# Performance work log

Hardware: AMD Instinct MI355X
Metric: run time of the kernel (lower is better)

## Reference

```python
import jax, jax.numpy as jnp
import numpy as np
import math

B, T, D_MODEL, N_HEADS, K_CONV = 2, 2048, 2048, 16, 4
HEAD_DIM = D_MODEL // N_HEADS
EPS_GN = 1e-5


def setup_inputs() -> dict:
    key = jax.random.key(0)
    ks = jax.random.split(key, 16)
    s = 0.02
    # gamma bias init per reset_parameters (decays 0.9..0.9999 per head)
    min_d, max_d = 0.9, 0.9999
    tgt = 1.0 - np.exp(np.linspace(math.log(1 - min_d), math.log(1 - max_d), N_HEADS))
    gamma_bias = np.log(tgt / (1 - tgt)).astype(np.float32)
    return {
        "x": jax.random.normal(ks[0], (B, T, D_MODEL), jnp.float32),
        "Wq": jax.random.normal(ks[1], (D_MODEL, D_MODEL), jnp.float32) * s,
        "Wk": jax.random.normal(ks[2], (D_MODEL, D_MODEL), jnp.float32) * s,
        "Wv": jax.random.normal(ks[3], (D_MODEL, D_MODEL), jnp.float32) * s,
        "Wo": jax.random.normal(ks[4], (D_MODEL, D_MODEL), jnp.float32) * s,
        "conv_w": jax.random.normal(ks[5], (D_MODEL, K_CONV), jnp.float32) * 0.1,
        "conv_b": jnp.zeros((D_MODEL,), jnp.float32),
        "Wig": jax.random.normal(ks[6], (D_MODEL, D_MODEL), jnp.float32) * s,
        "b_ig": jnp.zeros((D_MODEL,), jnp.float32),
        "Wog": jax.random.normal(ks[7], (D_MODEL, D_MODEL), jnp.float32) * s,
        "b_og": jnp.zeros((D_MODEL,), jnp.float32),
        "Wg": jnp.zeros((N_HEADS, D_MODEL), jnp.float32),
        "b_g": jnp.asarray(gamma_bias),
        "gn_w": jnp.ones((D_MODEL,), jnp.float32),
        "gn_b": jnp.zeros((D_MODEL,), jnp.float32),
        "mn_w": jnp.ones((D_MODEL,), jnp.float32),
        "mn_b": jnp.zeros((D_MODEL,), jnp.float32),
    }


def _group_norm(x2d, w, b, groups, eps):
    # x2d: [N, C], normalize per group of C//groups channels
    N, C = x2d.shape
    xg = x2d.reshape(N, groups, C // groups)
    mu = xg.mean(-1, keepdims=True)
    var = ((xg - mu) ** 2).mean(-1, keepdims=True)
    xn = ((xg - mu) * jax.lax.rsqrt(var + eps)).reshape(N, C)
    return xn * w + b


def _causal_depthwise_conv(x, w, b):
    # x: [B,T,C], w: [C,K], b: [C] -> [B,T,C] causal depthwise conv + silu
    xt = jnp.transpose(x, (0, 2, 1))  # [B,C,T]
    xp = jnp.pad(xt, ((0, 0), (0, 0), (K_CONV - 1, 0)))
    y = jax.lax.conv_general_dilated(
        xp, w[:, None, :], (1,), "VALID",
        feature_group_count=D_MODEL,
        dimension_numbers=("NCH", "OIH", "NCH"))
    y = y + b[None, :, None]
    return jax.nn.silu(jnp.transpose(y, (0, 2, 1)))


def _l2norm(t):
    n = jnp.sqrt(jnp.sum(t * t, axis=-1, keepdims=True))
    return t / jnp.maximum(n, 1e-12)


def reference(x, Wq, Wk, Wv, Wo, conv_w, conv_b, Wig, b_ig, Wog, b_og, Wg, b_g, gn_w, gn_b, mn_w, mn_b):
    Bq, Tq, C = x.shape
    x_conv = _causal_depthwise_conv(x, conv_w, conv_b)  # [B,T,C]

    q = _l2norm((x @ Wq.T).reshape(Bq, Tq, N_HEADS, HEAD_DIM))
    k = _l2norm((x @ Wk.T).reshape(Bq, Tq, N_HEADS, HEAD_DIM))
    v = (x @ Wv.T).reshape(Bq, Tq, N_HEADS, HEAD_DIM)

    input_gate = jax.nn.sigmoid(x_conv @ Wig.T + b_ig).reshape(Bq, Tq, N_HEADS, HEAD_DIM)
    gamma = jax.nn.sigmoid(x_conv @ Wg.T + b_g).reshape(Bq, Tq, N_HEADS, 1)

    # gated elementwise linear recurrence: h_t = gamma_t * h_{t-1} + i_t * (k_t * v_t)
    bterm = input_gate * k * v                       # [B,T,H,D]
    aterm = jnp.broadcast_to(gamma, bterm.shape)     # [B,T,H,D]

    def scan_op(c1, c2):
        a1, b1 = c1
        a2, b2 = c2
        return (a1 * a2, a2 * b1 + b2)

    _, mem = jax.lax.associative_scan(scan_op, (aterm, bterm), axis=1)
    next_rnn_state = mem[:, -1]

    mem_n = _group_norm(mem.reshape(Bq * Tq, D_MODEL), mn_w, mn_b, N_HEADS, EPS_GN)
    mem_n = mem_n.reshape(Bq, Tq, N_HEADS, HEAD_DIM)

    out = (mem_n * q).reshape(Bq * Tq, C)
    out = _group_norm(out, gn_w, gn_b, N_HEADS, EPS_GN).reshape(Bq, Tq, C)

    output_gate = jax.nn.sigmoid(x_conv @ Wog.T + b_og)
    out = (out * output_gate) @ Wo.T

    new_conv_cache = jnp.transpose(x, (0, 2, 1))[:, :, -(K_CONV - 1):]
    return out, next_rnn_state, new_conv_cache
```

## Files before the change

### kernel.cpp

```cpp
#include <hip/hip_runtime.h>
#include <math.h>

#define B_ 2
#define T_ 2048
#define D_ 2048
#define H_ 16
#define M_ 4096
#define TD_ (T_ * D_)
#define EPS_ 1e-5f
#define NC_ 64
#define CL_ 32

typedef __bf16 bf16x8 __attribute__((ext_vector_type(8)));
typedef float f32x4 __attribute__((ext_vector_type(4)));

__device__ __forceinline__ float sigm(float z) { return 1.f / (1.f + __expf(-z)); }

__device__ __forceinline__ ushort f2bf(float f) {
    union { float f; uint u; } x; x.f = f;
    uint r = x.u + 0x7fffu + ((x.u >> 16) & 1u);
    return (ushort)(r >> 16);
}
__device__ __forceinline__ float bflo(uint u) { union { uint u; float f; } x; x.u = u << 16; return x.f; }
__device__ __forceinline__ float bfhi(uint u) { union { uint u; float f; } x; x.u = u & 0xffff0000u; return x.f; }

__device__ __forceinline__ void gload_lds16(const void* g, void* l) {
    __builtin_amdgcn_global_load_lds((const __attribute__((address_space(1))) void*)g,
                                     (__attribute__((address_space(3))) void*)l, 16, 0, 0);
}

template <int IMM>
__device__ __forceinline__ bf16x8 dsr(uint addr) {
    int4 d;
    asm volatile("ds_read_b128 %0, %1 offset:%2" : "=v"(d) : "v"(addr), "n"(IMM));
    return __builtin_bit_cast(bf16x8, d);
}
#define SCB   __builtin_amdgcn_sched_barrier(0)
#define SBAR  __builtin_amdgcn_s_barrier()

__global__ __launch_bounds__(256) void cvtw_kernel(
    const float* __restrict__ Wq, const float* __restrict__ Wk, const float* __restrict__ Wv,
    const float* __restrict__ Wig, const float* __restrict__ Wog, const float* __restrict__ Wo,
    ushort* __restrict__ W6)
{
    const int z = blockIdx.y;
    const float* src = z == 0 ? Wq : z == 1 ? Wk : z == 2 ? Wv : z == 3 ? Wig : z == 4 ? Wog : Wo;
    const int i4 = (blockIdx.x * 256 + threadIdx.x) * 4;
    float4 f = *(const float4*)(src + i4);
    ushort4 o; o.x = f2bf(f.x); o.y = f2bf(f.y); o.z = f2bf(f.z); o.w = f2bf(f.w);
    *(ushort4*)(W6 + (size_t)z * ((size_t)D_ * D_) + i4) = o;
}

__global__ __launch_bounds__(256) void conv_kernel(
    const float* __restrict__ x, const float* __restrict__ cw, const float* __restrict__ cb,
    ushort* __restrict__ xb, ushort* __restrict__ xcb, float* __restrict__ cach)
{
    const int idx = blockIdx.x * 256 + threadIdx.x;
    const int c = idx & (D_ - 1);
    const int t = (idx >> 11) & (T_ - 1);
    const int b = idx >> 22;
    const float* w = cw + c * 4;
    const float x3 = x[idx];
    float a = cb[c] + w[3] * x3;
    if (t >= 1) a += w[2] * x[idx - D_];
    if (t >= 2) a += w[1] * x[idx - 2 * D_];
    if (t >= 3) a += w[0] * x[idx - 3 * D_];
    xb[idx] = f2bf(x3);
    xcb[idx] = f2bf(a * sigm(a));
    if (t >= T_ - 3) cach[((size_t)b * D_ + c) * 3 + (t - (T_ - 3))] = x3;
}

template <bool BF16OUT>
__device__ __forceinline__ void gemm256_body(
    const ushort* __restrict__ A, const ushort* __restrict__ Bw,
    ushort* __restrict__ Cb, float* __restrict__ Cf, int bx, int by)
{
    extern __shared__ char smem[];
    const int tid = threadIdx.x;
    const int lane = tid & 63, wid = tid >> 6;
    const int wm = wid >> 1, wn = wid & 1;
    const int l15 = lane & 15, l4 = lane >> 4;
    const int brow = by * 256, bcol = bx * 128;

    const int srow = tid >> 3;
    const int scol = ((tid & 7) * 8) ^ (((tid >> 3) & 7) << 3);
    const uint sldso = (uint)tid * 16;

    f32x4 acc[4][4] = {};

    #define STAGE6(bufo, k0)                                                         \
        do {                                                                         \
            _Pragma("unroll")                                                        \
            for (int j = 0; j < 4; ++j)                                              \
                gload_lds16(A + (size_t)(brow + j * 64 + srow) * D_ + ((k0) + scol), \
                            smem + (bufo) + j * 8192 + sldso);                       \
            _Pragma("unroll")                                                        \
            for (int j = 0; j < 2; ++j)                                              \
                gload_lds16(Bw + (size_t)(bcol + j * 64 + srow) * D_ + ((k0) + scol),\
                            smem + (bufo) + 32768u + j * 8192 + sldso);              \
        } while (0)

    STAGE6(0u, 0);
    STAGE6(49152u, 64);
    asm volatile("s_waitcnt vmcnt(6)" ::: "memory");
    SBAR; SCB;

    const uint r7  = (uint)((l15 & 7) << 4);
    const uint ca0 = (uint)(l4 * 16) ^ r7;
    const uint ca1 = (uint)(64 + l4 * 16) ^ r7;
    const uint arow = (uint)(wm * 64 + l15) * 128u;
    const uint brw  = 32768u + (uint)(wn * 64 + l15) * 128u;
    const uint ldsbase = (uint)(size_t)smem;

    #pragma unroll 2
    for (int t = 0; t < 32; ++t) {
        const uint bo = ldsbase + (uint)(t & 1) * 49152u;
        const uint ab0 = bo + arow + ca0, ab1 = bo + arow + ca1;
        const uint bb0 = bo + brw + ca0,  bb1 = bo + brw + ca1;
        bf16x8 a0[8], b0[4], b1[4];
        a0[0] = dsr<0>(ab0);        a0[1] = dsr<0>(ab1);
        a0[2] = dsr<2048>(ab0);     a0[3] = dsr<2048>(ab1);
        a0[4] = dsr<4096>(ab0);     a0[5] = dsr<4096>(ab1);
        a0[6] = dsr<6144>(ab0);     a0[7] = dsr<6144>(ab1);
        b0[0] = dsr<0>(bb0);        b0[1] = dsr<0>(bb1);
        b0[2] = dsr<2048>(bb0);     b0[3] = dsr<2048>(bb1);
        b1[0] = dsr<4096>(bb0);     b1[1] = dsr<4096>(bb1);
        b1[2] = dsr<6144>(bb0);     b1[3] = dsr<6144>(bb1);
        asm volatile("s_waitcnt lgkmcnt(4)" ::: "memory");
        SCB;
        __builtin_amdgcn_s_setprio(1);
        #pragma unroll
        for (int ks = 0; ks < 2; ++ks)
            #pragma unroll
            for (int m = 0; m < 4; ++m)
                #pragma unroll
                for (int n = 0; n < 2; ++n)
                    acc[m][n] = __builtin_amdgcn_mfma_f32_16x16x32_bf16(
                        a0[m * 2 + ks], b0[n * 2 + ks], acc[m][n], 0, 0, 0);
        SCB;
        __builtin_amdgcn_s_setprio(0);
        asm volatile("s_waitcnt lgkmcnt(0)" ::: "memory");
        SCB;
        __builtin_amdgcn_s_setprio(1);
        #pragma unroll
        for (int ks = 0; ks < 2; ++ks)
            #pragma unroll
            for (int m = 0; m < 4; ++m)
                #pragma unroll
                for (int n = 0; n < 2; ++n)
                    acc[m][2 + n] = __builtin_amdgcn_mfma_f32_16x16x32_bf16(
                        a0[m * 2 + ks], b1[n * 2 + ks], acc[m][2 + n], 0, 0, 0);
        SCB;
        __builtin_amdgcn_s_setprio(0);
        if (t <= 29) {
            const uint bo2 = (uint)(t & 1) * 49152u;
            STAGE6(bo2, (t + 2) * 64);
        }
        if (t < 31) {
            if (t < 30) asm volatile("s_waitcnt vmcnt(6)" ::: "memory");
            else        asm volatile("s_waitcnt vmcnt(0)" ::: "memory");
            SBAR; SCB;
        }
    }
    #undef STAGE6

    #pragma unroll
    for (int m = 0; m < 4; ++m)
        #pragma unroll
        for (int n = 0; n < 4; ++n) {
            const int row = brow + wm * 64 + m * 16 + l4 * 4;
            const int col = bcol + wn * 64 + n * 16 + l15;
            #pragma unroll
            for (int r = 0; r < 4; ++r) {
                if (BF16OUT) Cb[(size_t)(row + r) * D_ + col] = f2bf(acc[m][n][r]);
                else         Cf[(size_t)(row + r) * D_ + col] = acc[m][n][r];
            }
        }
}

__global__ __launch_bounds__(512, 2) void gemm5_kernel(
    const ushort* __restrict__ xb, const ushort* __restrict__ xcb,
    const ushort* __restrict__ W6, ushort* __restrict__ Obuf)
{
    const int g = (blockIdx.z * 16 + blockIdx.y) * 16 + blockIdx.x;
    const int ns = (g & 7) * 160 + (g >> 3);
    const int z = ns >> 8, rem = ns & 255, by = rem >> 4, bx = rem & 15;
    const ushort* Aop = (z < 3) ? xb : xcb;
    gemm256_body<true>(Aop, W6 + (size_t)z * ((size_t)D_ * D_),
                       Obuf + (size_t)z * ((size_t)M_ * D_), nullptr, bx, by);
}

__global__ __launch_bounds__(512, 2) void gemm_out_kernel(
    const ushort* __restrict__ gated, const ushort* __restrict__ W6, float* __restrict__ out)
{
    const int g = blockIdx.y * 16 + blockIdx.x;
    const int ns = (g & 7) * 32 + (g >> 3);
    const int by = ns >> 4, bx = ns & 15;
    gemm256_body<false>(gated, W6 + (size_t)5 * ((size_t)D_ * D_), nullptr, out, bx, by);
}

__global__ __launch_bounds__(256) void gamma_kernel(
    const ushort* __restrict__ xcb, const float* __restrict__ Wg,
    const float* __restrict__ bg, float* __restrict__ gamma)
{
    __shared__ ushort xs[8 * D_];
    const int tid = threadIdx.x;
    const int tok0 = blockIdx.x * 8;
    const uint4* gsrc = (const uint4*)(xcb + (size_t)tok0 * D_);
    #pragma unroll
    for (int j = 0; j < 8; ++j)
        ((uint4*)xs)[j * 256 + tid] = gsrc[j * 256 + tid];
    __syncthreads();
    const int tok = tid >> 5;
    const int h = (tid >> 1) & 15;
    const int half = tid & 1;
    const ushort* xr = xs + tok * D_ + half * 1024;
    const float* wr = Wg + (size_t)h * D_ + half * 1024;
    float acc = 0.f;
    #pragma unroll 4
    for (int i = 0; i < 1024; i += 8) {
        uint4 u = *(const uint4*)(xr + i);
        float4 w0 = *(const float4*)(wr + i);
        float4 w1 = *(const float4*)(wr + i + 4);
        acc += bflo(u.x) * w0.x + bfhi(u.x) * w0.y + bflo(u.y) * w0.z + bfhi(u.y) * w0.w;
        acc += bflo(u.z) * w1.x + bfhi(u.z) * w1.y + bflo(u.w) * w1.z + bfhi(u.w) * w1.w;
    }
    acc += __shfl_xor(acc, 1);
    if (!half) gamma[(size_t)(tok0 + tok) * H_ + h] = sigm(acc + bg[h]);
}

__global__ __launch_bounds__(64) void scanA_kernel(
    const ushort* __restrict__ kb, const ushort* __restrict__ vb,
    const ushort* __restrict__ igb, const float* __restrict__ big,
    const float* __restrict__ gam, float* __restrict__ Ab, float* __restrict__ Sb)
{
    const int l = threadIdx.x;
    const int ch = blockIdx.x, h = blockIdx.y, b = blockIdx.z;
    const int c0 = h * 128 + 2 * l;
    const float bg0 = big[c0], bg1 = big[c0 + 1];
    const float* g = gam + ((size_t)b * T_ + ch * CL_) * H_ + h;
    const size_t base0 = ((size_t)b * T_ + ch * CL_) * D_ + c0;
    float a = 1.f, sA = 0.f, sB = 0.f;
    for (int i = 0; i < CL_; ++i) {
        const size_t off = base0 + (size_t)i * D_;
        const uint ku = *(const uint*)(kb + off);
        const uint vu = *(const uint*)(vb + off);
        const uint iu = *(const uint*)(igb + off);
        const float k0 = bflo(ku), k1 = bfhi(ku);
        float ssq = k0 * k0 + k1 * k1;
        #pragma unroll
        for (int o = 1; o < 64; o <<= 1) ssq += __shfl_xor(ssq, o);
        const float sc = 1.f / fmaxf(sqrtf(ssq), 1e-12f);
        const float b0 = sigm(bflo(iu) + bg0) * (k0 * sc) * bflo(vu);
        const float b1 = sigm(bfhi(iu) + bg1) * (k1 * sc) * bfhi(vu);
        const float gv = g[(size_t)i * H_];
        sA = fmaf(gv, sA, b0);
        sB = fmaf(gv, sB, b1);
        a *= gv;
    }
    const size_t o = ((size_t)b * NC_ + ch) * D_ + c0;
    Ab[o] = a; Ab[o + 1] = a; Sb[o] = sA; Sb[o + 1] = sB;
}

__global__ __launch_bounds__(256) void scan2_kernel(
    const float* __restrict__ Ab, const float* __restrict__ Sb, float* __restrict__ carry)
{
    const int idx = blockIdx.x * 256 + threadIdx.x;
    const int b = idx >> 11, c = idx & (D_ - 1);
    float run = 0.f;
    #pragma unroll 8
    for (int ch = 0; ch < NC_; ++ch) {
        const size_t o = ((size_t)b * NC_ + ch) * D_ + c;
        carry[o] = run;
        run = fmaf(Ab[o], run, Sb[o]);
    }
}

__global__ __launch_bounds__(64) void scanB_kernel(
    const ushort* __restrict__ kb, const ushort* __restrict__ vb,
    const ushort* __restrict__ igb, const ushort* __restrict__ qb,
    const ushort* __restrict__ ogb, const float* __restrict__ big,
    const float* __restrict__ bog, const float* __restrict__ mnw,
    const float* __restrict__ mnb, const float* __restrict__ gnw,
    const float* __restrict__ gnb, const float* __restrict__ gam,
    const float* __restrict__ carry, ushort* __restrict__ gated,
    float* __restrict__ rnn)
{
    const int l = threadIdx.x;
    const int ch = blockIdx.x, h = blockIdx.y, b = blockIdx.z;
    const int c0 = h * 128 + 2 * l;
    const float bg0 = big[c0], bg1 = big[c0 + 1];
    const float bo0 = bog[c0], bo1 = bog[c0 + 1];
    const float mw0 = mnw[c0], mw1 = mnw[c0 + 1], mb0 = mnb[c0], mb1 = mnb[c0 + 1];
    const float gw0 = gnw[c0], gw1 = gnw[c0 + 1], gb0 = gnb[c0], gb1 = gnb[c0 + 1];
    const float* g = gam + ((size_t)b * T_ + ch * CL_) * H_ + h;
    const size_t base0 = ((size_t)b * T_ + ch * CL_) * D_ + c0;
    float m0 = carry[((size_t)b * NC_ + ch) * D_ + c0];
    float m1 = carry[((size_t)b * NC_ + ch) * D_ + c0 + 1];
    for (int i = 0; i < CL_; ++i) {
        const size_t off = base0 + (size_t)i * D_;
        const uint ku = *(const uint*)(kb + off);
        const uint vu = *(const uint*)(vb + off);
        const uint iu = *(const uint*)(igb + off);
        const uint qu = *(const uint*)(qb + off);
        const uint ou = *(const uint*)(ogb + off);
        const float k0 = bflo(ku), k1 = bfhi(ku);
        float ssq = k0 * k0 + k1 * k1;
        #pragma unroll
        for (int o = 1; o < 64; o <<= 1) ssq += __shfl_xor(ssq, o);
        const float sc = 1.f / fmaxf(sqrtf(ssq), 1e-12f);
        const float bt0 = sigm(bflo(iu) + bg0) * (k0 * sc) * bflo(vu);
        const float bt1 = sigm(bfhi(iu) + bg1) * (k1 * sc) * bfhi(vu);
        const float gv = g[(size_t)i * H_];
        m0 = fmaf(gv, m0, bt0);
        m1 = fmaf(gv, m1, bt1);
        const float q0 = bflo(qu), q1 = bfhi(qu);
        float r1 = m0 + m1, r2 = m0 * m0 + m1 * m1, r3 = q0 * q0 + q1 * q1;
        #pragma unroll
        for (int o = 1; o < 64; o <<= 1) {
            r1 += __shfl_xor(r1, o); r2 += __shfl_xor(r2, o); r3 += __shfl_xor(r3, o);
        }
        const float mu  = r1 * (1.f / 128.f);
        const float inv = 1.f / sqrtf(fmaxf(r2 * (1.f / 128.f) - mu * mu, 0.f) + EPS_);
        const float qsc = 1.f / fmaxf(sqrtf(r3), 1e-12f);
        const float ov0 = ((m0 - mu) * inv * mw0 + mb0) * (q0 * qsc);
        const float ov1 = ((m1 - mu) * inv * mw1 + mb1) * (q1 * qsc);
        float t1 = ov0 + ov1, t2 = ov0 * ov0 + ov1 * ov1;
        #pragma unroll
        for (int o = 1; o < 64; o <<= 1) { t1 += __shfl_xor(t1, o); t2 += __shfl_xor(t2, o); }
        const float mu2  = t1 * (1.f / 128.f);
        const float inv2 = 1.f / sqrtf(fmaxf(t2 * (1.f / 128.f) - mu2 * mu2, 0.f) + EPS_);
        const float g0 = ((ov0 - mu2) * inv2 * gw0 + gb0) * sigm(bflo(ou) + bo0);
        const float g1 = ((ov1 - mu2) * inv2 * gw1 + gb1) * sigm(bfhi(ou) + bo1);
        *(uint*)(gated + off) = (uint)f2bf(g0) | ((uint)f2bf(g1) << 16);
    }
    if (ch == NC_ - 1) {
        rnn[(size_t)b * D_ + c0] = m0;
        rnn[(size_t)b * D_ + c0 + 1] = m1;
    }
}

extern "C" void kernel_launch(void* const* d_in, const int* in_sizes, int n_in,
                              void* d_out, int out_size, void* d_ws, size_t ws_size,
                              hipStream_t stream)
{
    const float* x   = (const float*)d_in[0];
    const float* Wq  = (const float*)d_in[1];
    const float* Wk  = (const float*)d_in[2];
    const float* Wv  = (const float*)d_in[3];
    const float* Wo  = (const float*)d_in[4];
    const float* cw  = (const float*)d_in[5];
    const float* cb  = (const float*)d_in[6];
    const float* Wig = (const float*)d_in[7];
    const float* big = (const float*)d_in[8];
    const float* Wog = (const float*)d_in[9];
    const float* bog = (const float*)d_in[10];
    const float* Wg  = (const float*)d_in[11];
    const float* bg  = (const float*)d_in[12];
    const float* gnw = (const float*)d_in[13];
    const float* gnb = (const float*)d_in[14];
    const float* mnw = (const float*)d_in[15];
    const float* mnb = (const float*)d_in[16];

    char* ws = (char*)d_ws;
    ushort* W6   = (ushort*)ws;
    ushort* xb   = (ushort*)(ws + 50331648);
    ushort* xcb  = (ushort*)(ws + 50331648 + 16777216);
    ushort* Obuf = (ushort*)(ws + 50331648 + 2 * 16777216);
    float*  gam  = (float*)(ws + 167772160);
    ushort* gated= (ushort*)(ws + 167772160 + 1048576);
    float*  Ab   = (float*)(ws + 167772160 + 1048576 + 16777216);
    float*  Sb   = Ab + (size_t)B_ * NC_ * D_;
    float*  carry= Sb + (size_t)B_ * NC_ * D_;

    ushort* q    = Obuf;
    ushort* k    = Obuf + (size_t)M_ * D_;
    ushort* v    = Obuf + 2 * (size_t)M_ * D_;
    ushort* igp  = Obuf + 3 * (size_t)M_ * D_;
    ushort* ogp  = Obuf + 4 * (size_t)M_ * D_;

    float* out  = (float*)d_out;
    float* rnn  = out + (size_t)M_ * D_;
    float* cach = rnn + B_ * D_;

    (void)hipFuncSetAttribute((const void*)gemm5_kernel,
                              hipFuncAttributeMaxDynamicSharedMemorySize, 98304);
    (void)hipFuncSetAttribute((const void*)gemm_out_kernel,
                              hipFuncAttributeMaxDynamicSharedMemorySize, 98304);

    cvtw_kernel<<<dim3(4096, 6), 256, 0, stream>>>(Wq, Wk, Wv, Wig, Wog, Wo, W6);
    conv_kernel<<<dim3(M_ * D_ / 256), 256, 0, stream>>>(x, cw, cb, xb, xcb, cach);
    gemm5_kernel<<<dim3(16, 16, 5), 512, 98304, stream>>>(xb, xcb, W6, Obuf);
    gamma_kernel<<<dim3(M_ / 8), 256, 0, stream>>>(xcb, Wg, bg, gam);
    scanA_kernel<<<dim3(NC_, H_, B_), 64, 0, stream>>>(k, v, igp, big, gam, Ab, Sb);
    scan2_kernel<<<dim3(16), 256, 0, stream>>>(Ab, Sb, carry);
    scanB_kernel<<<dim3(NC_, H_, B_), 64, 0, stream>>>(k, v, igp, q, ogp, big, bog,
                                                       mnw, mnb, gnw, gnb, gam, carry,
                                                       gated, rnn);
    gemm_out_kernel<<<dim3(16, 16), 512, 98304, stream>>>(gated, W6, out);
}
```

Measured before the change: 416.3 us.

## Vectorize scan kernels to 8 channels per lane and shorten scan chunks

Each lane in the chunked-scan kernels now handles 8 contiguous channels with 128-bit bf16 loads and stores, and a wave covers 4 heads with 16-lane shuffle reductions instead of 64-lane ones. Chunk length drops from 32 to 8, giving 256 chunks. The per-chunk decay/state buffer is interleaved as float2 and stored channel-major. Workspace regions freed by earlier stages (xb, W6) are reused for the scan buffers and the gated output. The aim is fewer, wider memory transactions and shorter reduction chains, at the cost of a 4x longer serial carry pass in scan2, which now reads with strided, poorly coalesced access.

```diff
diff --git a/kernel.cpp b/kernel.cpp
--- a/kernel.cpp
+++ b/kernel.cpp
@@ -8,8 +8,8 @@
 #define M_ 4096
 #define TD_ (T_ * D_)
 #define EPS_ 1e-5f
-#define NC_ 64
-#define CL_ 32
+#define NC_ 256
+#define CL_ 8
 
 typedef __bf16 bf16x8 __attribute__((ext_vector_type(8)));
 typedef float f32x4 __attribute__((ext_vector_type(4)));
@@ -23,6 +23,13 @@
 }
 __device__ __forceinline__ float bflo(uint u) { union { uint u; float f; } x; x.u = u << 16; return x.f; }
 __device__ __forceinline__ float bfhi(uint u) { union { uint u; float f; } x; x.u = u & 0xffff0000u; return x.f; }
+
+__device__ __forceinline__ void unp8(uint4 u, float* f) {
+    f[0] = bflo(u.x); f[1] = bfhi(u.x); f[2] = bflo(u.y); f[3] = bfhi(u.y);
+    f[4] = bflo(u.z); f[5] = bfhi(u.z); f[6] = bflo(u.w); f[7] = bfhi(u.w);
+}
+#define RED16(v) do { v += __shfl_xor(v, 1); v += __shfl_xor(v, 2); \
+                      v += __shfl_xor(v, 4); v += __shfl_xor(v, 8); } while (0)
 
 __device__ __forceinline__ void gload_lds16(const void* g, void* l) {
     __builtin_amdgcn_global_load_lds((const __attribute__((address_space(1))) void*)g,
@@ -232,47 +239,55 @@
 __global__ __launch_bounds__(64) void scanA_kernel(
     const ushort* __restrict__ kb, const ushort* __restrict__ vb,
     const ushort* __restrict__ igb, const float* __restrict__ big,
-    const float* __restrict__ gam, float* __restrict__ Ab, float* __restrict__ Sb)
+    const float* __restrict__ gam, float2* __restrict__ AS)
 {
     const int l = threadIdx.x;
-    const int ch = blockIdx.x, h = blockIdx.y, b = blockIdx.z;
-    const int c0 = h * 128 + 2 * l;
-    const float bg0 = big[c0], bg1 = big[c0 + 1];
+    const int ch = blockIdx.x, hg = blockIdx.y, b = blockIdx.z;
+    const int h = hg * 4 + (l >> 4);
+    const int c0 = h * 128 + (l & 15) * 8;
+    float bg[8];
+    #pragma unroll
+    for (int j = 0; j < 8; ++j) bg[j] = big[c0 + j];
     const float* g = gam + ((size_t)b * T_ + ch * CL_) * H_ + h;
-    const size_t base0 = ((size_t)b * T_ + ch * CL_) * D_ + c0;
-    float a = 1.f, sA = 0.f, sB = 0.f;
+    const size_t base = ((size_t)b * T_ + ch * CL_) * D_ + c0;
+    float a = 1.f, s[8] = {};
+    #pragma unroll
     for (int i = 0; i < CL_; ++i) {
-        const size_t off = base0 + (size_t)i * D_;
-        const uint ku = *(const uint*)(kb + off);
-        const uint vu = *(const uint*)(vb + off);
-        const uint iu = *(const uint*)(igb + off);
-        const float k0 = bflo(ku), k1 = bfhi(ku);
-        float ssq = k0 * k0 + k1 * k1;
-        #pragma unroll
-        for (int o = 1; o < 64; o <<= 1) ssq += __shfl_xor(ssq, o);
+        const size_t off = base + (size_t)i * D_;
+        uint4 ku = *(const uint4*)(kb + off);
+        uint4 vu = *(const uint4*)(vb + off);
+        uint4 iu = *(const uint4*)(igb + off);
+        float kf[8], vf[8], gf[8];
+        unp8(ku, kf); unp8(vu, vf); unp8(iu, gf);
+        float ssq = 0.f;
+        #pragma unroll
+        for (int j = 0; j < 8; ++j) ssq += kf[j] * kf[j];
+        RED16(ssq);
         const float sc = 1.f / fmaxf(sqrtf(ssq), 1e-12f);
-        const float b0 = sigm(bflo(iu) + bg0) * (k0 * sc) * bflo(vu);
-        const float b1 = sigm(bfhi(iu) + bg1) * (k1 * sc) * bfhi(vu);
         const float gv = g[(size_t)i * H_];
-        sA = fmaf(gv, sA, b0);
-        sB = fmaf(gv, sB, b1);
         a *= gv;
-    }
-    const size_t o = ((size_t)b * NC_ + ch) * D_ + c0;
-    Ab[o] = a; Ab[o + 1] = a; Sb[o] = sA; Sb[o + 1] = sB;
+        #pragma unroll
+        for (int j = 0; j < 8; ++j)
+            s[j] = fmaf(gv, s[j], sigm(gf[j] + bg[j]) * (kf[j] * sc) * vf[j]);
+    }
+    #pragma unroll
+    for (int j = 0; j < 8; ++j) {
+        float2 as2; as2.x = a; as2.y = s[j];
+        AS[((size_t)b * D_ + c0 + j) * NC_ + ch] = as2;
+    }
 }
 
 __global__ __launch_bounds__(256) void scan2_kernel(
-    const float* __restrict__ Ab, const float* __restrict__ Sb, float* __restrict__ carry)
+    const float2* __restrict__ AS, float* __restrict__ carry)
 {
     const int idx = blockIdx.x * 256 + threadIdx.x;
-    const int b = idx >> 11, c = idx & (D_ - 1);
+    const size_t base = (size_t)idx * NC_;
     float run = 0.f;
     #pragma unroll 8
     for (int ch = 0; ch < NC_; ++ch) {
-        const size_t o = ((size_t)b * NC_ + ch) * D_ + c;
-        carry[o] = run;
-        run = fmaf(Ab[o], run, Sb[o]);
+        const float2 as2 = AS[base + ch];
+        carry[base + ch] = run;
+        run = fmaf(as2.x, run, as2.y);
     }
 }
 
@@ -287,56 +302,71 @@
     float* __restrict__ rnn)
 {
     const int l = threadIdx.x;
-    const int ch = blockIdx.x, h = blockIdx.y, b = blockIdx.z;
-    const int c0 = h * 128 + 2 * l;
-    const float bg0 = big[c0], bg1 = big[c0 + 1];
-    const float bo0 = bog[c0], bo1 = bog[c0 + 1];
-    const float mw0 = mnw[c0], mw1 = mnw[c0 + 1], mb0 = mnb[c0], mb1 = mnb[c0 + 1];
-    const float gw0 = gnw[c0], gw1 = gnw[c0 + 1], gb0 = gnb[c0], gb1 = gnb[c0 + 1];
+    const int ch = blockIdx.x, hg = blockIdx.y, b = blockIdx.z;
+    const int h = hg * 4 + (l >> 4);
+    const int c0 = h * 128 + (l & 15) * 8;
+    float bg[8], bo[8], mw[8], mb[8], gw[8], gb[8];
+    #pragma unroll
+    for (int j = 0; j < 8; ++j) {
+        bg[j] = big[c0 + j]; bo[j] = bog[c0 + j];
+        mw[j] = mnw[c0 + j]; mb[j] = mnb[c0 + j];
+        gw[j] = gnw[c0 + j]; gb[j] = gnb[c0 + j];
+    }
     const float* g = gam + ((size_t)b * T_ + ch * CL_) * H_ + h;
-    const size_t base0 = ((size_t)b * T_ + ch * CL_) * D_ + c0;
-    float m0 = carry[((size_t)b * NC_ + ch) * D_ + c0];
-    float m1 = carry[((size_t)b * NC_ + ch) * D_ + c0 + 1];
+    const size_t base = ((size_t)b * T_ + ch * CL_) * D_ + c0;
+    float m[8];
+    #pragma unroll
+    for (int j = 0; j < 8; ++j) m[j] = carry[((size_t)b * D_ + c0 + j) * NC_ + ch];
+    #pragma unroll
     for (int i = 0; i < CL_; ++i) {
-        const size_t off = base0 + (size_t)i * D_;
-        const uint ku = *(const uint*)(kb + off);
-        const uint vu = *(const uint*)(vb + off);
-        const uint iu = *(const uint*)(igb + off);
-        const uint qu = *(const uint*)(qb + off);
-        const uint ou = *(const uint*)(ogb + off);
-        const float k0 = bflo(ku), k1 = bfhi(ku);
-        float ssq = k0 * k0 + k1 * k1;
-        #pragma unroll
-        for (int o = 1; o < 64; o <<= 1) ssq += __shfl_xor(ssq, o);
+        const size_t off = base + (size_t)i * D_;
+        uint4 ku = *(const uint4*)(kb + off);
+        uint4 vu = *(const uint4*)(vb + off);
+        uint4 iu = *(const uint4*)(igb + off);
+        uint4 qu = *(const uint4*)(qb + off);
+        uint4 ou = *(const uint4*)(ogb + off);
+        float kf[8], vf[8], gf[8], qf[8], of[8];
+        unp8(ku, kf); unp8(vu, vf); unp8(iu, gf); unp8(qu, qf); unp8(ou, of);
+        float ssq = 0.f;
+        #pragma unroll
+        for (int j = 0; j < 8; ++j) ssq += kf[j] * kf[j];
+        RED16(ssq);
         const float sc = 1.f / fmaxf(sqrtf(ssq), 1e-12f);
-        const float bt0 = sigm(bflo(iu) + bg0) * (k0 * sc) * bflo(vu);
-        const float bt1 = sigm(bfhi(iu) + bg1) * (k1 * sc) * bfhi(vu);
         const float gv = g[(size_t)i * H_];
-        m0 = fmaf(gv, m0, bt0);
-        m1 = fmaf(gv, m1, bt1);
-        const float q0 = bflo(qu), q1 = bfhi(qu);
-        float r1 = m0 + m1, r2 = m0 * m0 + m1 * m1, r3 = q0 * q0 + q1 * q1;
-        #pragma unroll
-        for (int o = 1; o < 64; o <<= 1) {
-            r1 += __shfl_xor(r1, o); r2 += __shfl_xor(r2, o); r3 += __shfl_xor(r3, o);
-        }
+        #pragma unroll
+        for (int j = 0; j < 8; ++j)
+            m[j] = fmaf(gv, m[j], sigm(gf[j] + bg[j]) * (kf[j] * sc) * vf[j]);
+        float r1 = 0.f, r2 = 0.f, r3 = 0.f;
+        #pragma unroll
+        for (int j = 0; j < 8; ++j) { r1 += m[j]; r2 += m[j] * m[j]; r3 += qf[j] * qf[j]; }
+        RED16(r1); RED16(r2); RED16(r3);
         const float mu  = r1 * (1.f / 128.f);
         const float inv = 1.f / sqrtf(fmaxf(r2 * (1.f / 128.f) - mu * mu, 0.f) + EPS_);
         const float qsc = 1.f / fmaxf(sqrtf(r3), 1e-12f);
-        const float ov0 = ((m0 - mu) * inv * mw0 + mb0) * (q0 * qsc);
-        const float ov1 = ((m1 - mu) * inv * mw1 + mb1) * (q1 * qsc);
-        float t1 = ov0 + ov1, t2 = ov0 * ov0 + ov1 * ov1;
-        #pragma unroll
-        for (int o = 1; o < 64; o <<= 1) { t1 += __shfl_xor(t1, o); t2 += __shfl_xor(t2, o); }
+        float ov[8]; float t1 = 0.f, t2 = 0.f;
+        #pragma unroll
+        for (int j = 0; j < 8; ++j) {
+            ov[j] = ((m[j] - mu) * inv * mw[j] + mb[j]) * (qf[j] * qsc);
+            t1 += ov[j]; t2 += ov[j] * ov[j];
+        }
+        RED16(t1); RED16(t2);
         const float mu2  = t1 * (1.f / 128.f);
         const float inv2 = 1.f / sqrtf(fmaxf(t2 * (1.f / 128.f) - mu2 * mu2, 0.f) + EPS_);
-        const float g0 = ((ov0 - mu2) * inv2 * gw0 + gb0) * sigm(bflo(ou) + bo0);
-        const float g1 = ((ov1 - mu2) * inv2 * gw1 + gb1) * sigm(bfhi(ou) + bo1);
-        *(uint*)(gated + off) = (uint)f2bf(g0) | ((uint)f2bf(g1) << 16);
+        uint pk[4];
+        #pragma unroll
+        for (int j2 = 0; j2 < 4; ++j2) {
+            const float g0 = ((ov[2*j2]   - mu2) * inv2 * gw[2*j2]   + gb[2*j2])   * sigm(of[2*j2]   + bo[2*j2]);
+            const float g1 = ((ov[2*j2+1] - mu2) * inv2 * gw[2*j2+1] + gb[2*j2+1]) * sigm(of[2*j2+1] + bo[2*j2+1]);
+            pk[j2] = (uint)f2bf(g0) | ((uint)f2bf(g1) << 16);
+        }
+        uint4 st = { pk[0], pk[1], pk[2], pk[3] };
+        *(uint4*)(gated + off) = st;
     }
     if (ch == NC_ - 1) {
-        rnn[(size_t)b * D_ + c0] = m0;
-        rnn[(size_t)b * D_ + c0 + 1] = m1;
+        float* r = rnn + (size_t)b * D_ + c0;
+        float4 r0 = { m[0], m[1], m[2], m[3] };
+        float4 r1v = { m[4], m[5], m[6], m[7] };
+        *(float4*)r = r0; *(float4*)(r + 4) = r1v;
     }
 }
 
@@ -368,10 +398,6 @@
     ushort* xcb  = (ushort*)(ws + 50331648 + 16777216);
     ushort* Obuf = (ushort*)(ws + 50331648 + 2 * 16777216);
     float*  gam  = (float*)(ws + 167772160);
-    ushort* gated= (ushort*)(ws + 167772160 + 1048576);
-    float*  Ab   = (float*)(ws + 167772160 + 1048576 + 16777216);
-    float*  Sb   = Ab + (size_t)B_ * NC_ * D_;
-    float*  carry= Sb + (size_t)B_ * NC_ * D_;
 
     ushort* q    = Obuf;
     ushort* k    = Obuf + (size_t)M_ * D_;
@@ -379,6 +405,10 @@
     ushort* igp  = Obuf + 3 * (size_t)M_ * D_;
     ushort* ogp  = Obuf + 4 * (size_t)M_ * D_;
 
+    float2* AS    = (float2*)xb;
+    float*  carry = (float*)(ws + 50331648 + 8388608);
+    ushort* gated = W6;
+
     float* out  = (float*)d_out;
     float* rnn  = out + (size_t)M_ * D_;
     float* cach = rnn + B_ * D_;
@@ -392,10 +422,10 @@
     conv_kernel<<<dim3(M_ * D_ / 256), 256, 0, stream>>>(x, cw, cb, xb, xcb, cach);
     gemm5_kernel<<<dim3(16, 16, 5), 512, 98304, stream>>>(xb, xcb, W6, Obuf);
     gamma_kernel<<<dim3(M_ / 8), 256, 0, stream>>>(xcb, Wg, bg, gam);
-    scanA_kernel<<<dim3(NC_, H_, B_), 64, 0, stream>>>(k, v, igp, big, gam, Ab, Sb);
-    scan2_kernel<<<dim3(16), 256, 0, stream>>>(Ab, Sb, carry);
-    scanB_kernel<<<dim3(NC_, H_, B_), 64, 0, stream>>>(k, v, igp, q, ogp, big, bog,
-                                                       mnw, mnb, gnw, gnb, gam, carry,
-                                                       gated, rnn);
+    scanA_kernel<<<dim3(NC_, 4, B_), 64, 0, stream>>>(k, v, igp, big, gam, AS);
+    scan2_kernel<<<dim3(B_ * D_ / 256), 256, 0, stream>>>(AS, carry);
+    scanB_kernel<<<dim3(NC_, 4, B_), 64, 0, stream>>>(k, v, igp, q, ogp, big, bog,
+                                                      mnw, mnb, gnw, gnb, gam, carry,
+                                                      gated, rnn);
     gemm_out_kernel<<<dim3(16, 16), 512, 98304, stream>>>(gated, W6, out);
 }
```

Measured after the change: 419.7 us. Within noise of the previous version (+0.8%).
